# Performance work log

Measured on AMD Instinct MI355X. Metric: run time of the kernel, lower is better.

The kernel has to match this reference:

```python
import jax, jax.numpy as jnp
import numpy as np

B, N, F_IN, F_OUT = 32, 1024, 256, 256
K_NEIGHBORS = 64
TEMPERATURE = 1.0
LN_EPS = 1e-5


def setup_inputs() -> dict:
    key = jax.random.key(0)
    ks = jax.random.split(key, 10)
    s_in = 1.0 / np.sqrt(F_IN)
    s_out = 1.0 / np.sqrt(F_OUT)
    # learned static adjacency: 0.1 everywhere + 0.9 on diagonal (self loops)
    static_edge_weights = jnp.full((N, N), 0.1, dtype=jnp.float32) + 0.9 * jnp.eye(N, dtype=jnp.float32)
    return {
        "x": jax.random.normal(ks[0], (B, N, F_IN), dtype=jnp.float32),
        "wq": jax.random.uniform(ks[1], (F_IN, F_OUT), jnp.float32, -s_in, s_in),
        "bq": jnp.zeros((F_OUT,), jnp.float32),
        "wk": jax.random.uniform(ks[2], (F_IN, F_OUT), jnp.float32, -s_in, s_in),
        "bk": jnp.zeros((F_OUT,), jnp.float32),
        "wv": jax.random.uniform(ks[3], (F_IN, F_OUT), jnp.float32, -s_in, s_in),
        "bv": jnp.zeros((F_OUT,), jnp.float32),
        "static_edge_weights": static_edge_weights,
        "w1": jax.random.uniform(ks[4], (F_OUT, F_OUT), jnp.float32, -s_out, s_out),
        "b1": jnp.zeros((F_OUT,), jnp.float32),
        "ln_g": jnp.ones((F_OUT,), jnp.float32),
        "ln_b": jnp.zeros((F_OUT,), jnp.float32),
        "w2": jax.random.uniform(ks[5], (F_OUT, F_OUT), jnp.float32, -s_out, s_out),
        "b2": jnp.zeros((F_OUT,), jnp.float32),
    }


def reference(x, wq, bq, wk, bk, wv, bv, static_edge_weights, w1, b1, ln_g, ln_b, w2, b2):
    Bc, Nc, _ = x.shape
    q = jnp.einsum("bnf,fo->bno", x, wq) + bq
    k = jnp.einsum("bnf,fo->bno", x, wk) + bk
    v = jnp.einsum("bnf,fo->bno", x, wv) + bv
    # [B, N, N] attention scores with learned static adjacency bias
    scores = jnp.einsum("bnd,bmd->bnm", q, k) / jnp.sqrt(jnp.float32(F_OUT))
    scores = scores + static_edge_weights[None, :, :]
    # top-k sparsification along last dim
    _, topk_idx = jax.lax.top_k(scores, K_NEIGHBORS)  # [B, N, K]
    bi = jnp.arange(Bc)[:, None, None]
    ni = jnp.arange(Nc)[None, :, None]
    mask = jnp.zeros(scores.shape, dtype=bool).at[bi, ni, topk_idx].set(True)
    scores = jnp.where(mask, scores, jnp.float32(-1e9))
    attn = jax.nn.softmax(scores / TEMPERATURE, axis=-1)
    messages = jnp.einsum("bnm,bmd->bnd", attn, v)
    # out_mlp: Linear -> LayerNorm -> ReLU -> Linear
    h = jnp.einsum("bnd,de->bne", messages, w1) + b1
    mu = jnp.mean(h, axis=-1, keepdims=True)
    var = jnp.mean(jnp.square(h - mu), axis=-1, keepdims=True)
    h = (h - mu) / jnp.sqrt(var + LN_EPS) * ln_g + ln_b
    h = jax.nn.relu(h)
    h = jnp.einsum("bnd,de->bne", h, w2) + b2
    out = h + v  # residual
    return (out, attn)
```

## Files before the change

kernel.cpp:

```cpp
#include <hip/hip_runtime.h>
#include <cstdint>

#define NB 32
#define NNODES 1024
#define DD 256
#define KNB 64
#define MTOT (NB * NNODES)

#define INV65536 1.52587890625e-05f
#define KCELL 2.44140625e-4f

typedef _Float16 half8 __attribute__((ext_vector_type(8)));
typedef _Float16 half4 __attribute__((ext_vector_type(4)));
typedef float f32x4 __attribute__((ext_vector_type(4)));

typedef __attribute__((address_space(3))) uint32_t lds_u32;
typedef __attribute__((address_space(1))) uint32_t glb_u32;

__device__ __forceinline__ void gll16(const _Float16* g, _Float16* l) {
  __builtin_amdgcn_global_load_lds((const glb_u32*)g, (lds_u32*)l, 16, 0, 0);
}

__device__ __forceinline__ void split2(float v, _Float16& h, _Float16& l) {
  h = (_Float16)v;
  l = (_Float16)(v - (float)h);
}

__global__ __launch_bounds__(256) void prep_w(const float* __restrict__ wq,
                                              const float* __restrict__ wk,
                                              const float* __restrict__ wv,
                                              const float* __restrict__ w1,
                                              const float* __restrict__ w2,
                                              _Float16* __restrict__ WT) {
  const int idx = blockIdx.x * 256 + threadIdx.x;
  const int wsel = idx >> 16;
  const int rem = idx & 65535;
  const int k = rem >> 8, n = rem & 255;
  const float* src = (wsel == 0) ? wq : (wsel == 1) ? wk : (wsel == 2) ? wv : (wsel == 3) ? w1 : w2;
  const float v = src[rem] * 1024.0f;
  _Float16 h1, h2;
  split2(v, h1, h2);
  WT[(size_t)wsel * 131072 + n * 256 + k] = h1;
  WT[(size_t)wsel * 131072 + 65536 + n * 256 + k] = h2;
}

__global__ __launch_bounds__(256) void prep_x(const float* __restrict__ x,
                                              _Float16* __restrict__ X1,
                                              _Float16* __restrict__ X2) {
  const size_t i = ((size_t)blockIdx.x * 256 + threadIdx.x) * 8;
  const float4 a = *(const float4*)(x + i);
  const float4 bb = *(const float4*)(x + i + 4);
  const float vals[8] = {a.x, a.y, a.z, a.w, bb.x, bb.y, bb.z, bb.w};
  half8 h, l;
#pragma unroll
  for (int e = 0; e < 8; ++e) {
    _Float16 hh, ll;
    split2(vals[e] * 64.0f, hh, ll);
    h[e] = hh;
    l[e] = ll;
  }
  *(half8*)(X1 + i) = h;
  *(half8*)(X2 + i) = l;
}

#define SWZ_OFF(r, cc) ((r) * 64 + (((cc) ^ ((r)&7)) << 3))

__global__ __launch_bounds__(256) void gemm_qkv(const _Float16* __restrict__ X1,
                                                const _Float16* __restrict__ X2,
                                                const _Float16* __restrict__ WT,
                                                const float* __restrict__ bq,
                                                const float* __restrict__ bk,
                                                const float* __restrict__ bv,
                                                _Float16* __restrict__ Q1, _Float16* __restrict__ Q2,
                                                _Float16* __restrict__ K1, _Float16* __restrict__ K2,
                                                _Float16* __restrict__ V16) {
  __shared__ _Float16 sm[4 * 8192];
  _Float16* sA1 = sm;
  _Float16* sA2 = sm + 8192;
  _Float16* sB1 = sm + 16384;
  _Float16* sB2 = sm + 24576;

  const int tid = threadIdx.x;
  const int lane = tid & 63, w = tid >> 6;
  const int r16 = lane & 15, kg = lane >> 4;
  const int rsub = lane >> 3, csub = lane & 7;
  const int wm = (w >> 1) * 64, wn = (w & 1) * 64;

  const int id = blockIdx.x;
  const int c8 = id & 7, t = id >> 3;
  const int gy = (t / 6) * 8 + c8;
  const int j6 = t % 6;
  const int wsel = j6 >> 1;
  const int n0 = (j6 & 1) * 128;
  const int m0 = gy * 128;
  const bool full = (wsel != 2);

  const _Float16* pB1 = WT + (size_t)wsel * 131072;
  const _Float16* pB2 = pB1 + 65536;

  f32x4 acc[4][4];
#pragma unroll
  for (int i = 0; i < 4; ++i)
#pragma unroll
    for (int j = 0; j < 4; ++j) acc[i][j] = f32x4{0.f, 0.f, 0.f, 0.f};

  for (int k0 = 0; k0 < DD; k0 += 64) {
    __syncthreads();
#pragma unroll
    for (int it = 0; it < 4; ++it) {
      const int r = (w << 5) + (it << 3) + rsub;
      const int swz = ((csub ^ (r & 7)) << 3);
      const int ldso = (w << 11) + (it << 9);
      gll16(X1 + (size_t)(m0 + r) * DD + k0 + swz, sA1 + ldso);
      gll16(pB1 + (size_t)(n0 + r) * DD + k0 + swz, sB1 + ldso);
      if (full) {
        gll16(X2 + (size_t)(m0 + r) * DD + k0 + swz, sA2 + ldso);
        gll16(pB2 + (size_t)(n0 + r) * DD + k0 + swz, sB2 + ldso);
      }
    }
    __syncthreads();

#pragma unroll
    for (int s = 0; s < 2; ++s) {
      half8 aA[4], aB[4], bA[4], bB[4];
#pragma unroll
      for (int mi = 0; mi < 4; ++mi) {
        const int off = SWZ_OFF(wm + mi * 16 + r16, s * 4 + kg);
        aA[mi] = *(const half8*)(sA1 + off);
      }
#pragma unroll
      for (int nj = 0; nj < 4; ++nj) {
        const int off = SWZ_OFF(wn + nj * 16 + r16, s * 4 + kg);
        bA[nj] = *(const half8*)(sB1 + off);
      }
      if (full) {
#pragma unroll
        for (int mi = 0; mi < 4; ++mi) {
          const int off = SWZ_OFF(wm + mi * 16 + r16, s * 4 + kg);
          aB[mi] = *(const half8*)(sA2 + off);
        }
#pragma unroll
        for (int nj = 0; nj < 4; ++nj) {
          const int off = SWZ_OFF(wn + nj * 16 + r16, s * 4 + kg);
          bB[nj] = *(const half8*)(sB2 + off);
        }
      }
#pragma unroll
      for (int mi = 0; mi < 4; ++mi)
#pragma unroll
        for (int nj = 0; nj < 4; ++nj) {
          acc[mi][nj] = __builtin_amdgcn_mfma_f32_16x16x32_f16(aA[mi], bA[nj], acc[mi][nj], 0, 0, 0);
          if (full) {
            acc[mi][nj] = __builtin_amdgcn_mfma_f32_16x16x32_f16(aA[mi], bB[nj], acc[mi][nj], 0, 0, 0);
            acc[mi][nj] = __builtin_amdgcn_mfma_f32_16x16x32_f16(aB[mi], bA[nj], acc[mi][nj], 0, 0, 0);
          }
        }
    }
  }

  const float* bsel = (wsel == 0) ? bq : (wsel == 1) ? bk : bv;
  _Float16* P1 = (wsel == 0) ? Q1 : K1;
  _Float16* P2 = (wsel == 0) ? Q2 : K2;
#pragma unroll
  for (int mi = 0; mi < 4; ++mi)
#pragma unroll
    for (int nj = 0; nj < 4; ++nj) {
      const int col = n0 + wn + nj * 16 + r16;
#pragma unroll
      for (int j = 0; j < 4; ++j) {
        const int rr = m0 + wm + mi * 16 + kg * 4 + j;
        if (wsel == 2) {
          V16[(size_t)rr * DD + col] = (_Float16)(acc[mi][nj][j] * INV65536 + bsel[col]);
        } else {
          const float qv = acc[mi][nj][j] * (1.0f / 1024.0f) + 64.0f * bsel[col];
          _Float16 h1, h2;
          split2(qv, h1, h2);
          P1[(size_t)rr * DD + col] = h1;
          P2[(size_t)rr * DD + col] = h2;
        }
      }
    }
}

template <int EPI>
__global__ __launch_bounds__(256) void gemm_split(const _Float16* __restrict__ A1,
                                                  const _Float16* __restrict__ B1g,
                                                  const _Float16* __restrict__ B2g,
                                                  const float* __restrict__ bias,
                                                  const _Float16* __restrict__ resid16,
                                                  float* __restrict__ C) {
  __shared__ _Float16 sm[3 * 8192];
  _Float16* sA1 = sm;
  _Float16* sB1 = sm + 8192;
  _Float16* sB2 = sm + 16384;

  const int tid = threadIdx.x;
  const int lane = tid & 63, w = tid >> 6;
  const int r16 = lane & 15, kg = lane >> 4;
  const int rsub = lane >> 3, csub = lane & 7;
  const int wm = (w >> 1) * 64, wn = (w & 1) * 64;

  const int n0 = blockIdx.x * 128;
  const int m0 = blockIdx.y * 128;

  const _Float16* pB1 = B1g;
  const _Float16* pB2 = B2g;
  if (EPI == 2) {
    const size_t boff = (size_t)(m0 >> 10) * NNODES * DD;
    pB1 += boff;
    pB2 += boff;
  }

  f32x4 acc[4][4];
#pragma unroll
  for (int i = 0; i < 4; ++i)
#pragma unroll
    for (int j = 0; j < 4; ++j) acc[i][j] = f32x4{0.f, 0.f, 0.f, 0.f};

  for (int k0 = 0; k0 < DD; k0 += 64) {
    __syncthreads();
#pragma unroll
    for (int it = 0; it < 4; ++it) {
      const int r = (w << 5) + (it << 3) + rsub;
      const int swz = ((csub ^ (r & 7)) << 3);
      const int ldso = (w << 11) + (it << 9);
      gll16(A1 + (size_t)(m0 + r) * DD + k0 + swz, sA1 + ldso);
      gll16(pB1 + (size_t)(n0 + r) * DD + k0 + swz, sB1 + ldso);
      gll16(pB2 + (size_t)(n0 + r) * DD + k0 + swz, sB2 + ldso);
    }
    __syncthreads();

#pragma unroll
    for (int s = 0; s < 2; ++s) {
      half8 aA[4], bA[4], bB[4];
#pragma unroll
      for (int mi = 0; mi < 4; ++mi) {
        const int off = SWZ_OFF(wm + mi * 16 + r16, s * 4 + kg);
        aA[mi] = *(const half8*)(sA1 + off);
      }
#pragma unroll
      for (int nj = 0; nj < 4; ++nj) {
        const int off = SWZ_OFF(wn + nj * 16 + r16, s * 4 + kg);
        bA[nj] = *(const half8*)(sB1 + off);
        bB[nj] = *(const half8*)(sB2 + off);
      }
#pragma unroll
      for (int mi = 0; mi < 4; ++mi)
#pragma unroll
        for (int nj = 0; nj < 4; ++nj) {
          acc[mi][nj] = __builtin_amdgcn_mfma_f32_16x16x32_f16(aA[mi], bA[nj], acc[mi][nj], 0, 0, 0);
          acc[mi][nj] = __builtin_amdgcn_mfma_f32_16x16x32_f16(aA[mi], bB[nj], acc[mi][nj], 0, 0, 0);
        }
    }
  }

#pragma unroll
  for (int mi = 0; mi < 4; ++mi)
#pragma unroll
    for (int nj = 0; nj < 4; ++nj) {
      const int col = n0 + wn + nj * 16 + r16;
#pragma unroll
      for (int j = 0; j < 4; ++j) {
        const int rr = m0 + wm + mi * 16 + kg * 4 + j;
        const float v = acc[mi][nj][j] * INV65536;
        if (EPI == 2) {
          const float sv = v + bias[(size_t)(rr & (NNODES - 1)) * NNODES + col];
          const float f = fminf(fmaxf((sv + 8.0f) * 4096.0f, 0.0f), 65535.0f);
          uint16_t* kbase = (uint16_t*)((char*)C + (size_t)rr * 4096 + 2048);
          kbase[col] = (uint16_t)(unsigned)f;
        } else if (EPI == 0) {
          C[(size_t)rr * DD + col] = v + bias[col];
        } else {
          C[(size_t)rr * DD + col] = v + bias[col] + (float)resid16[(size_t)rr * DD + col];
        }
      }
    }
}

__global__ __launch_bounds__(256, 4) void topk_softmax_msg(float* __restrict__ S,
                                                           const _Float16* __restrict__ V16,
                                                           const _Float16* __restrict__ Q1,
                                                           const _Float16* __restrict__ Q2,
                                                           const _Float16* __restrict__ K1,
                                                           const _Float16* __restrict__ K2,
                                                           const float* __restrict__ adj,
                                                           _Float16* __restrict__ M1) {
  const int tid = threadIdx.x;
  const int w = tid >> 6, lane = tid & 63;
  const int id = blockIdx.x;
  const int xcd = id & 7, t = id >> 3;
  const int b = (t >> 8) * 8 + xcd;
  const int row = b * NNODES + (t & 255) * 4 + w;
  const int m = row & (NNODES - 1);
  float* Srow = S + (size_t)row * NNODES;
  const uint16_t* krow = (const uint16_t*)((const char*)S + (size_t)row * 4096 + 2048);

  __shared__ float2 spair[4][KNB];
  __shared__ int cidxs[4][32];
  __shared__ float cex[4][32];
  __shared__ int csel[4][32];

  if (lane < KNB) spair[w][lane] = make_float2(0.0f, __int_as_float(0));

  const uint4 u0 = *(const uint4*)(krow + lane * 8);
  const uint4 u1 = *(const uint4*)(krow + 512 + lane * 8);
  int k[16];
  {
    const unsigned uu[8] = {u0.x, u0.y, u0.z, u0.w, u1.x, u1.y, u1.z, u1.w};
#pragma unroll
    for (int q = 0; q < 8; ++q) {
      k[q * 2] = (int)(uu[q] & 0xffffu);
      k[q * 2 + 1] = (int)(uu[q] >> 16);
    }
  }

  float st[16];
#pragma unroll
  for (int t2 = 0; t2 < 16; ++t2) st[t2] = fmaf((float)k[t2] + 0.5f, KCELL, -8.0f);

  int cur = 0;
#pragma unroll 1
  for (int bit = 15; bit >= 0; --bit) {
    const int cand = cur | (1 << bit);
    int cnt = 0;
#pragma unroll
    for (int t2 = 0; t2 < 16; ++t2) cnt += (int)__popcll(__ballot(k[t2] >= cand));
    if (cnt >= KNB) cur = cand;
  }

  const int kHi = cur + 17;
  const int kLo = cur - 16;

  const unsigned long long ltmask = (1ull << lane) - 1ull;
  unsigned hm = 0u, cm = 0u;
  int cpos[16];
  int nhi = 0, ncand = 0;
#pragma unroll
  for (int g = 0; g < 2; ++g) {
    bool hiv[8], cdv[8];
    unsigned long long mh[8], mc[8];
#pragma unroll
    for (int e = 0; e < 8; ++e) {
      const int t2 = g * 8 + e;
      hiv[e] = (k[t2] >= kHi);
      cdv[e] = (!hiv[e]) && (k[t2] >= kLo);
      mh[e] = __ballot(hiv[e]);
      mc[e] = __ballot(cdv[e]);
    }
    int below = 0, tot_h = 0, tot_c = 0;
#pragma unroll
    for (int e = 0; e < 8; ++e) {
      below += (int)__popcll(mc[e] & ltmask);
      tot_h += (int)__popcll(mh[e]);
      tot_c += (int)__popcll(mc[e]);
    }
    int own = 0;
#pragma unroll
    for (int e = 0; e < 8; ++e) {
      const int t2 = g * 8 + e;
      cpos[t2] = -1;
      if (hiv[e]) hm |= (1u << t2);
      if (cdv[e]) {
        cm |= (1u << t2);
        const int p = ncand + below + own;
        cpos[t2] = p;
        if (p < 32) cidxs[w][p] = g * 512 + lane * 8 + e;
        ++own;
      }
    }
    nhi += tot_h;
    ncand += tot_c;
  }
  const int need = KNB - nhi;

  unsigned selm;
  if (ncand == need) {
    selm = hm | cm;
  } else {
    const int nc = (ncand <= 32) ? ncand : 32;
    const int nd = (need <= nc) ? need : nc;
    const size_t qoff = (size_t)row * DD + lane * 4;
    const half4 q1v = *(const half4*)(Q1 + qoff);
    const half4 q2v = *(const half4*)(Q2 + qoff);
    float qf[4];
#pragma unroll
    for (int e = 0; e < 4; ++e) qf[e] = (float)q1v[e] + (float)q2v[e];
    const float* adjrow = adj + (size_t)m * NNODES;
#pragma unroll 1
    for (int t2 = 0; t2 < nc; ++t2) {
      const int j = cidxs[w][t2];
      const size_t koff = ((size_t)b * NNODES + j) * DD + lane * 4;
      const half4 k1v = *(const half4*)(K1 + koff);
      const half4 k2v = *(const half4*)(K2 + koff);
      float part = 0.0f;
#pragma unroll
      for (int e = 0; e < 4; ++e) part = fmaf(qf[e], (float)k1v[e] + (float)k2v[e], part);
#pragma unroll
      for (int off = 32; off > 0; off >>= 1) part += __shfl_xor(part, off);
      if (lane == 0) cex[w][t2] = part * INV65536 + adjrow[j];
    }
    if (lane < nc) {
      const float et = cex[w][lane];
      int rank = 0;
      for (int u = 0; u < nc; ++u) {
        const float eu = cex[w][u];
        rank += (eu > et || (eu == et && u < lane)) ? 1 : 0;
      }
      csel[w][lane] = (rank < nd) ? 1 : 0;
    }
    selm = hm;
#pragma unroll
    for (int t2 = 0; t2 < 16; ++t2) {
      if (((cm >> t2) & 1u) && cpos[t2] >= 0 && cpos[t2] < 32 && csel[w][cpos[t2]]) selm |= (1u << t2);
    }
  }

  float rmax = st[0];
#pragma unroll
  for (int t2 = 1; t2 < 16; ++t2) rmax = fmaxf(rmax, st[t2]);
#pragma unroll
  for (int off = 32; off > 0; off >>= 1) rmax = fmaxf(rmax, __shfl_xor(rmax, off));

  float p[16];
  float sum = 0.0f;
#pragma unroll
  for (int t2 = 0; t2 < 16; ++t2) {
    p[t2] = __expf(st[t2] - rmax);
    if ((selm >> t2) & 1u) sum += p[t2];
  }
#pragma unroll
  for (int off = 32; off > 0; off >>= 1) sum += __shfl_xor(sum, off);
  const float inv = 1.0f / sum;

  int run = 0;
#pragma unroll
  for (int g = 0; g < 2; ++g) {
    bool sel8[8];
    unsigned long long ms[8];
#pragma unroll
    for (int e = 0; e < 8; ++e) {
      sel8[e] = (selm >> (g * 8 + e)) & 1u;
      ms[e] = __ballot(sel8[e]);
    }
    int below = 0, tot = 0;
#pragma unroll
    for (int e = 0; e < 8; ++e) {
      below += (int)__popcll(ms[e] & ltmask);
      tot += (int)__popcll(ms[e]);
    }
    float ow[8];
    int own = 0;
#pragma unroll
    for (int e = 0; e < 8; ++e) {
      const int t2 = g * 8 + e;
      const float aw = sel8[e] ? p[t2] * inv : 0.0f;
      ow[e] = aw;
      if (sel8[e]) {
        const int pos = run + below + own;
        if (pos < KNB)
          spair[w][pos] = make_float2(aw, __int_as_float((g * 512 + lane * 8 + e) * (DD * 2)));
        ++own;
      }
    }
    float* dst = Srow + g * 512 + lane * 8;
    *(float4*)(dst) = make_float4(ow[0], ow[1], ow[2], ow[3]);
    *(float4*)(dst + 4) = make_float4(ow[4], ow[5], ow[6], ow[7]);
    run += tot;
  }

  float4 acc = {0.0f, 0.0f, 0.0f, 0.0f};
  const char* Vbase = (const char*)(V16 + (size_t)b * NNODES * DD) + lane * 8;
#pragma unroll 4
  for (int t2 = 0; t2 < KNB; ++t2) {
    const float2 pr = spair[w][t2];
    const int off = __float_as_int(pr.y);
    const half4 vv = *(const half4*)(Vbase + off);
    acc.x = fmaf(pr.x, (float)vv[0], acc.x);
    acc.y = fmaf(pr.x, (float)vv[1], acc.y);
    acc.z = fmaf(pr.x, (float)vv[2], acc.z);
    acc.w = fmaf(pr.x, (float)vv[3], acc.w);
  }
  half4 m1;
  m1[0] = (_Float16)(acc.x * 64.0f);
  m1[1] = (_Float16)(acc.y * 64.0f);
  m1[2] = (_Float16)(acc.z * 64.0f);
  m1[3] = (_Float16)(acc.w * 64.0f);
  *(half4*)(M1 + (size_t)row * DD + lane * 4) = m1;
}

__global__ __launch_bounds__(256) void ln_relu(const float* __restrict__ H,
                                               const float* __restrict__ g,
                                               const float* __restrict__ bta,
                                               _Float16* __restrict__ H1) {
  const int row = blockIdx.x;
  const int c = threadIdx.x;
  const int wv = c >> 6, ln = c & 63;
  const float h = H[(size_t)row * DD + c];

  __shared__ float part[4], part2[4];
  float v = h;
#pragma unroll
  for (int off = 32; off > 0; off >>= 1) v += __shfl_xor(v, off);
  if (ln == 0) part[wv] = v;
  __syncthreads();
  const float mu = (part[0] + part[1] + part[2] + part[3]) * (1.0f / 256.0f);

  const float d = h - mu;
  float sq = d * d;
#pragma unroll
  for (int off = 32; off > 0; off >>= 1) sq += __shfl_xor(sq, off);
  if (ln == 0) part2[wv] = sq;
  __syncthreads();
  const float var = (part2[0] + part2[1] + part2[2] + part2[3]) * (1.0f / 256.0f);

  const float y = fmaxf(d * (1.0f / sqrtf(var + 1e-5f)) * g[c] + bta[c], 0.0f);
  H1[(size_t)row * DD + c] = (_Float16)(y * 64.0f);
}

extern "C" void kernel_launch(void* const* d_in, const int* in_sizes, int n_in,
                              void* d_out, int out_size, void* d_ws, size_t ws_size,
                              hipStream_t stream) {
  (void)in_sizes; (void)n_in; (void)out_size; (void)ws_size;
  const float* x   = (const float*)d_in[0];
  const float* wq  = (const float*)d_in[1];
  const float* bq  = (const float*)d_in[2];
  const float* wk  = (const float*)d_in[3];
  const float* bk  = (const float*)d_in[4];
  const float* wv  = (const float*)d_in[5];
  const float* bv  = (const float*)d_in[6];
  const float* adj = (const float*)d_in[7];
  const float* w1  = (const float*)d_in[8];
  const float* b1  = (const float*)d_in[9];
  const float* lng = (const float*)d_in[10];
  const float* lnb = (const float*)d_in[11];
  const float* w2  = (const float*)d_in[12];
  const float* b2  = (const float*)d_in[13];

  const size_t BND = (size_t)MTOT * DD;
  float* outp  = (float*)d_out;
  float* attnp = outp + BND;

  _Float16* X1 = (_Float16*)attnp;
  _Float16* X2 = X1 + BND;

  _Float16* Q1 = (_Float16*)d_ws;
  _Float16* Q2 = Q1 + BND;
  _Float16* K1 = Q2 + BND;
  _Float16* K2 = K1 + BND;
  _Float16* WT = K2 + BND;
  _Float16* V16 = WT + 5 * 131072;

  _Float16* M1 = Q1;
  float* H = (float*)K1;
  _Float16* H1 = Q1;

  const dim3 blk(256);

  prep_w<<<dim3(1280), blk, 0, stream>>>(wq, wk, wv, w1, w2, WT);
  prep_x<<<dim3(4096), blk, 0, stream>>>(x, X1, X2);
  gemm_qkv<<<dim3(1536), blk, 0, stream>>>(X1, X2, WT, bq, bk, bv, Q1, Q2, K1, K2, V16);
  gemm_split<2><<<dim3(8, 256), blk, 0, stream>>>(Q1, K1, K2, adj, nullptr, attnp);
  topk_softmax_msg<<<dim3(MTOT / 4), blk, 0, stream>>>(attnp, V16, Q1, Q2, K1, K2, adj, M1);
  gemm_split<0><<<dim3(2, 256), blk, 0, stream>>>(M1, WT + 3 * 131072, WT + 3 * 131072 + 65536,
                                                  b1, nullptr, H);
  ln_relu<<<dim3(MTOT), blk, 0, stream>>>(H, lng, lnb, H1);
  gemm_split<1><<<dim3(2, 256), blk, 0, stream>>>(H1, WT + 4 * 131072, WT + 4 * 131072 + 65536,
                                                  b2, V16, outp);
}
```

Baseline: 333.8 us.

## Store hidden activations as fp16, narrow top-k candidate band, vectorize LayerNorm

The first MLP GEMM now writes its output as fp16 rather than fp32, halving that intermediate's traffic, and LayerNorm reads it as half4 with one wave per row, using shuffles instead of LDS reductions and barriers. The top-k refinement band around the radix threshold shrinks from ±16 to ±4 quantization cells, so fewer candidates need exact rescoring, and the rescoring loop is unrolled by two. The narrower band risks misselecting elements near the k-th value when quantized scores are close, and fp16 storage of the pre-LayerNorm activations loses precision.

```diff
diff --git a/kernel.cpp b/kernel.cpp
--- a/kernel.cpp
+++ b/kernel.cpp
@@ -188,7 +188,8 @@
                                                   const _Float16* __restrict__ B2g,
                                                   const float* __restrict__ bias,
                                                   const _Float16* __restrict__ resid16,
-                                                  float* __restrict__ C) {
+                                                  float* __restrict__ C,
+                                                  _Float16* __restrict__ C16) {
   __shared__ _Float16 sm[3 * 8192];
   _Float16* sA1 = sm;
   _Float16* sB1 = sm + 8192;
@@ -269,7 +270,7 @@
           uint16_t* kbase = (uint16_t*)((char*)C + (size_t)rr * 4096 + 2048);
           kbase[col] = (uint16_t)(unsigned)f;
         } else if (EPI == 0) {
-          C[(size_t)rr * DD + col] = v + bias[col];
+          C16[(size_t)rr * DD + col] = (_Float16)(v + bias[col]);
         } else {
           C[(size_t)rr * DD + col] = v + bias[col] + (float)resid16[(size_t)rr * DD + col];
         }
@@ -328,8 +329,8 @@
     if (cnt >= KNB) cur = cand;
   }
 
-  const int kHi = cur + 17;
-  const int kLo = cur - 16;
+  const int kHi = cur + 5;
+  const int kLo = cur - 4;
 
   const unsigned long long ltmask = (1ull << lane) - 1ull;
   unsigned hm = 0u, cm = 0u;
@@ -386,7 +387,7 @@
 #pragma unroll
     for (int e = 0; e < 4; ++e) qf[e] = (float)q1v[e] + (float)q2v[e];
     const float* adjrow = adj + (size_t)m * NNODES;
-#pragma unroll 1
+#pragma unroll 2
     for (int t2 = 0; t2 < nc; ++t2) {
       const int j = cidxs[w][t2];
       const size_t koff = ((size_t)b * NNODES + j) * DD + lane * 4;
@@ -488,33 +489,44 @@
   *(half4*)(M1 + (size_t)row * DD + lane * 4) = m1;
 }
 
-__global__ __launch_bounds__(256) void ln_relu(const float* __restrict__ H,
+__global__ __launch_bounds__(256) void ln_relu(const _Float16* __restrict__ H16,
                                                const float* __restrict__ g,
                                                const float* __restrict__ bta,
                                                _Float16* __restrict__ H1) {
-  const int row = blockIdx.x;
-  const int c = threadIdx.x;
-  const int wv = c >> 6, ln = c & 63;
-  const float h = H[(size_t)row * DD + c];
-
-  __shared__ float part[4], part2[4];
-  float v = h;
-#pragma unroll
-  for (int off = 32; off > 0; off >>= 1) v += __shfl_xor(v, off);
-  if (ln == 0) part[wv] = v;
-  __syncthreads();
-  const float mu = (part[0] + part[1] + part[2] + part[3]) * (1.0f / 256.0f);
-
-  const float d = h - mu;
-  float sq = d * d;
+  const int tid = threadIdx.x;
+  const int row = blockIdx.x * 4 + (tid >> 6);
+  const int lane = tid & 63;
+  const half4 hv = *(const half4*)(H16 + (size_t)row * DD + lane * 4);
+  float h[4];
+#pragma unroll
+  for (int j = 0; j < 4; ++j) h[j] = (float)hv[j];
+
+  float s = h[0] + h[1] + h[2] + h[3];
+#pragma unroll
+  for (int off = 32; off > 0; off >>= 1) s += __shfl_xor(s, off);
+  const float mu = s * (1.0f / 256.0f);
+
+  float d[4], sq = 0.0f;
+#pragma unroll
+  for (int j = 0; j < 4; ++j) {
+    d[j] = h[j] - mu;
+    sq += d[j] * d[j];
+  }
 #pragma unroll
   for (int off = 32; off > 0; off >>= 1) sq += __shfl_xor(sq, off);
-  if (ln == 0) part2[wv] = sq;
-  __syncthreads();
-  const float var = (part2[0] + part2[1] + part2[2] + part2[3]) * (1.0f / 256.0f);
-
-  const float y = fmaxf(d * (1.0f / sqrtf(var + 1e-5f)) * g[c] + bta[c], 0.0f);
-  H1[(size_t)row * DD + c] = (_Float16)(y * 64.0f);
+  const float rstd = 1.0f / sqrtf(sq * (1.0f / 256.0f) + 1e-5f);
+
+  const float4 gv = *(const float4*)(g + lane * 4);
+  const float4 bv = *(const float4*)(bta + lane * 4);
+  const float gg[4] = {gv.x, gv.y, gv.z, gv.w};
+  const float bb[4] = {bv.x, bv.y, bv.z, bv.w};
+  half4 o;
+#pragma unroll
+  for (int j = 0; j < 4; ++j) {
+    const float y = fmaxf(d[j] * rstd * gg[j] + bb[j], 0.0f);
+    o[j] = (_Float16)(y * 64.0f);
+  }
+  *(half4*)(H1 + (size_t)row * DD + lane * 4) = o;
 }
 
 extern "C" void kernel_launch(void* const* d_in, const int* in_sizes, int n_in,
@@ -551,7 +563,7 @@
   _Float16* V16 = WT + 5 * 131072;
 
   _Float16* M1 = Q1;
-  float* H = (float*)K1;
+  _Float16* H16 = (_Float16*)K1;
   _Float16* H1 = Q1;
 
   const dim3 blk(256);
@@ -559,11 +571,11 @@
   prep_w<<<dim3(1280), blk, 0, stream>>>(wq, wk, wv, w1, w2, WT);
   prep_x<<<dim3(4096), blk, 0, stream>>>(x, X1, X2);
   gemm_qkv<<<dim3(1536), blk, 0, stream>>>(X1, X2, WT, bq, bk, bv, Q1, Q2, K1, K2, V16);
-  gemm_split<2><<<dim3(8, 256), blk, 0, stream>>>(Q1, K1, K2, adj, nullptr, attnp);
+  gemm_split<2><<<dim3(8, 256), blk, 0, stream>>>(Q1, K1, K2, adj, nullptr, attnp, nullptr);
   topk_softmax_msg<<<dim3(MTOT / 4), blk, 0, stream>>>(attnp, V16, Q1, Q2, K1, K2, adj, M1);
   gemm_split<0><<<dim3(2, 256), blk, 0, stream>>>(M1, WT + 3 * 131072, WT + 3 * 131072 + 65536,
-                                                  b1, nullptr, H);
-  ln_relu<<<dim3(MTOT), blk, 0, stream>>>(H, lng, lnb, H1);
+                                                  b1, nullptr, nullptr, H16);
+  ln_relu<<<dim3(MTOT / 4), blk, 0, stream>>>(H16, lng, lnb, H1);
   gemm_split<1><<<dim3(2, 256), blk, 0, stream>>>(H1, WT + 4 * 131072, WT + 4 * 131072 + 65536,
-                                                  b2, V16, outp);
-}
+                                                  b2, V16, outp, nullptr);
+}
```

Measured after the change: 304.7 us. 1.1x faster.
